# Kernel tuning notes

Hardware: AMD Instinct MI355X
Metric: run time of the kernel (lower is better)

## Reference

```python
import jax, jax.numpy as jnp
import numpy as np

# ---- dims ----
B, NP_, NL = 32, 350, 30          # graphs, protein atoms, ligand atoms per graph
NG = NP_ + NL
N = B * NG                        # 12160 nodes
E = B * NP_ * NL                  # 336000 edges (dense bipartite per graph)
HID, HEADS, G = 128, 16, 20
DH = HID // HEADS
KV = 2 * HID + G                  # 276
R_MIN, R_MAX = 0.0, 10.0


def _mlp_params(key, din, dout, hid=HID):
    k1, k2 = jax.random.split(key)
    return (jax.random.normal(k1, (din, hid), jnp.float32) / np.sqrt(din),
            jnp.zeros((hid,), jnp.float32),
            jnp.ones((hid,), jnp.float32),
            jnp.zeros((hid,), jnp.float32),
            jax.random.normal(k2, (hid, dout), jnp.float32) / np.sqrt(hid),
            jnp.zeros((dout,), jnp.float32))


def setup_inputs() -> dict:
    key = jax.random.key(0)
    h = jax.random.normal(jax.random.fold_in(key, 0), (N, HID), jnp.float32)
    x = jax.random.normal(jax.random.fold_in(key, 1), (N, 3), jnp.float32) * 3.0
    # node layout per graph: NP_ protein atoms then NL ligand atoms
    mask_ligand = np.tile(np.concatenate([np.zeros(NP_, np.int64), np.ones(NL, np.int64)]), B)
    base = (np.arange(B) * NG)[:, None]
    prot = base + np.arange(NP_)[None, :]            # [B, NP_]
    lig = base + NP_ + np.arange(NL)[None, :]        # [B, NL]
    # torch: dst = repeat_interleave(protein, NL); src = ligand.repeat(NP_)
    dst = np.repeat(prot, NL, axis=1).reshape(-1)
    src = np.tile(lig, (1, NP_)).reshape(-1)
    inp = {"h": h, "x": x, "src": jnp.asarray(src), "dst": jnp.asarray(dst),
           "mask_ligand": jnp.asarray(mask_ligand)}
    dims = {"hk": (KV, HID), "hv": (KV, HID), "xv": (KV, HEADS), "hq": (HID, HID), "no": (2 * HID, HID)}
    for i, (nm, (di, do)) in enumerate(dims.items()):
        for s, arr in zip(("w1", "b1", "g", "be", "w2", "b2"), _mlp_params(jax.random.fold_in(key, 10 + i), di, do)):
            inp[f"{nm}_{s}"] = arr
    return inp


def _mlp(t, w1, b1, g, be, w2, b2):
    # Linear -> LayerNorm -> ReLU -> Linear
    y = t @ w1 + b1
    mu = y.mean(-1, keepdims=True)
    var = ((y - mu) ** 2).mean(-1, keepdims=True)
    y = jax.nn.relu((y - mu) * jax.lax.rsqrt(var + 1e-5) * g + be)
    return y @ w2 + b2


def _forward(h, x, src, dst, mask_ligand, ps):
    rel_x = x[src] - x[dst]                                   # [E,3]
    dist = jnp.linalg.norm(rel_x, axis=-1, keepdims=True)     # [E,1]
    offset = jnp.linspace(R_MIN, R_MAX, G)
    coeff = -0.5 / (offset[1] - offset[0]) ** 2
    r_feat = jnp.exp(coeff * (dist - offset) ** 2)            # [E,G]; outer_product(v) == v
    # inner layer unpacks (dst_i, src_i) = (src, dst): hi=h[src_i]=h[dst], hj=h[dst_i]=h[src]
    kv = jnp.concatenate([r_feat, h[dst], h[src]], -1)        # [E,KV]
    k = _mlp(kv, *ps["hk"]).reshape(-1, HEADS, DH)            # [E,H,dh]
    q = _mlp(h, *ps["hq"]).reshape(-1, HEADS, DH)             # [N,H,dh]
    logits = (q[src] * k).sum(-1) / np.sqrt(DH)               # [E,H]
    # scatter_softmax over dst_i = src groups (ligand nodes)
    smax = jax.ops.segment_max(logits, src, num_segments=N)
    ex = jnp.exp(logits - smax[src])
    alpha = ex / jax.ops.segment_sum(ex, src, num_segments=N)[src]   # [E,H]
    v = _mlp(kv, *ps["hv"]).reshape(-1, HEADS, DH)            # [E,H,dh]
    xv = _mlp(kv, *ps["xv"])                                  # [E,H]
    m = alpha[:, :, None] * v                                 # [E,H,dh]
    mx = (alpha * xv)[:, :, None] * rel_x[:, None, :]         # [E,H,3]
    out = jax.ops.segment_sum(m, src, num_segments=N).reshape(N, HID)
    out_x = jax.ops.segment_sum(mx, src, num_segments=N)      # [N,H,3]
    # out_fc: h_in[mask_ligand] with int64 mask gathers rows 0/1 (faithful to source)
    out = _mlp(jnp.concatenate([out, h[mask_ligand]], -1), *ps["no"])
    h_out = out + h
    x_out = x + out_x.mean(1)
    return h_out, x_out


def reference(h, x, src, dst, mask_ligand,
              hk_w1, hk_b1, hk_g, hk_be, hk_w2, hk_b2,
              hv_w1, hv_b1, hv_g, hv_be, hv_w2, hv_b2,
              xv_w1, xv_b1, xv_g, xv_be, xv_w2, xv_b2,
              hq_w1, hq_b1, hq_g, hq_be, hq_w2, hq_b2,
              no_w1, no_b1, no_g, no_be, no_w2, no_b2):
    ps = {"hk": (hk_w1, hk_b1, hk_g, hk_be, hk_w2, hk_b2),
          "hv": (hv_w1, hv_b1, hv_g, hv_be, hv_w2, hv_b2),
          "xv": (xv_w1, xv_b1, xv_g, xv_be, xv_w2, xv_b2),
          "hq": (hq_w1, hq_b1, hq_g, hq_be, hq_w2, hq_b2),
          "no": (no_w1, no_b1, no_g, no_be, no_w2, no_b2)}
    return _forward(h, x, src, dst, mask_ligand, ps)
```

## Files before the change

kernel.cpp:

```cpp
#include <hip/hip_runtime.h>
#include <math.h>

namespace {
constexpr int kB = 32;
constexpr int kNP = 350;
constexpr int kNL = 30;
constexpr int kNG = 380;
constexpr int kN = kB * kNG;
constexpr int kG = 20;
constexpr int kNPROT = kB * kNP;
constexpr int kNLIG = kB * kNL;
constexpr int TP = 32;
constexpr int NT = 11;
}

__global__ __launch_bounds__(256) void pre_kernel(
    const float* __restrict__ h,
    const float* __restrict__ wk1, const float* __restrict__ bk1,
    const float* __restrict__ wv1, const float* __restrict__ bv1,
    const float* __restrict__ wx1, const float* __restrict__ bx1,
    float* __restrict__ outKd, float* __restrict__ outVd, float* __restrict__ outXd,
    float* __restrict__ outKs, float* __restrict__ outVs, float* __restrict__ outXs) {
  const int m = blockIdx.y;
  const float* w1 = (m == 0) ? wk1 : (m == 1) ? wv1 : wx1;
  const float* b1 = (m == 0) ? bk1 : (m == 1) ? bv1 : bx1;
  const bool isProt = (blockIdx.x < 175);
  const int rbase = isProt ? blockIdx.x * 64 : (blockIdx.x - 175) * 64;
  float* outArr = isProt ? ((m == 0) ? outKd : (m == 1) ? outVd : outXd)
                         : ((m == 0) ? outKs : (m == 1) ? outVs : outXs);
  const float* wb = w1 + (isProt ? 20 * 128 : 148 * 128);

  __shared__ float sh[64 * 132];
  const int t = threadIdx.x;
#pragma unroll
  for (int j = 0; j < 8; ++j) {
    int flat = t + j * 256;
    int row = flat >> 5;
    int col = (flat & 31) * 4;
    int r = rbase + row;
    int node;
    if (isProt) node = (r / kNP) * kNG + (r % kNP);
    else        node = (r / kNL) * kNG + kNP + (r % kNL);
    *(float4*)&sh[row * 132 + col] = *(const float4*)(h + (size_t)node * 128 + col);
  }
  __syncthreads();

  const int dcol = (t & 31) * 4;
  const int rrow = (t >> 5) * 8;
  float4 acc[8];
#pragma unroll
  for (int i = 0; i < 8; ++i) acc[i] = make_float4(0.f, 0.f, 0.f, 0.f);

  for (int k = 0; k < 128; k += 4) {
    float4 a4[8];
#pragma unroll
    for (int i = 0; i < 8; ++i) a4[i] = *(float4*)&sh[(rrow + i) * 132 + k];
#pragma unroll
    for (int kk = 0; kk < 4; ++kk) {
      float4 w4 = *(const float4*)(wb + (size_t)(k + kk) * 128 + dcol);
#pragma unroll
      for (int i = 0; i < 8; ++i) {
        float a = (kk == 0) ? a4[i].x : (kk == 1) ? a4[i].y : (kk == 2) ? a4[i].z : a4[i].w;
        acc[i].x += a * w4.x; acc[i].y += a * w4.y;
        acc[i].z += a * w4.z; acc[i].w += a * w4.w;
      }
    }
  }
  float4 bias = make_float4(0.f, 0.f, 0.f, 0.f);
  if (!isProt) bias = *(const float4*)(b1 + dcol);
#pragma unroll
  for (int i = 0; i < 8; ++i) {
    float4 o = acc[i];
    o.x += bias.x; o.y += bias.y; o.z += bias.z; o.w += bias.w;
    *(float4*)(outArr + (size_t)(rbase + rrow + i) * 128 + dcol) = o;
  }
}

__global__ __launch_bounds__(128) void cvec_kernel(
    const float* __restrict__ h,
    const float* __restrict__ no_w1, const float* __restrict__ no_b1,
    const float* __restrict__ no_g, const float* __restrict__ no_be,
    const float* __restrict__ no_w2, const float* __restrict__ no_b2,
    float* __restrict__ cvec) {
  __shared__ float sy[128];
  __shared__ float sa[128];
  __shared__ float red[2];
  const int d = threadIdx.x;
  float y = no_b1[d];
  for (int i = 0; i < 128; ++i) y += h[i] * no_w1[(size_t)(128 + i) * 128 + d];
  sy[d] = y;
  __syncthreads();
  if (d == 0) {
    float s = 0.f, ss = 0.f;
    for (int i = 0; i < 128; ++i) { s += sy[i]; ss += sy[i] * sy[i]; }
    float mu = s / 128.f;
    red[0] = mu;
    red[1] = rsqrtf(ss / 128.f - mu * mu + 1e-5f);
  }
  __syncthreads();
  float a = (y - red[0]) * red[1] * no_g[d] + no_be[d];
  sa[d] = fmaxf(a, 0.f);
  __syncthreads();
  float o = no_b2[d];
  for (int i = 0; i < 128; ++i) o += sa[i] * no_w2[(size_t)i * 128 + d];
  cvec[d] = o;
}

__global__ __launch_bounds__(256) void prot_kernel(
    const float* __restrict__ h, const float* __restrict__ x,
    const float* __restrict__ cvec, float* __restrict__ hout, float* __restrict__ xout) {
  int idx = blockIdx.x * 256 + threadIdx.x;
  if (idx < kNPROT * 32) {
    int r = idx >> 5, c4 = (idx & 31) * 4;
    int node = (r / kNP) * kNG + (r % kNP);
    float4 hv = *(const float4*)(h + (size_t)node * 128 + c4);
    float4 cv = *(const float4*)(cvec + c4);
    *(float4*)(hout + (size_t)node * 128 + c4) =
        make_float4(hv.x + cv.x, hv.y + cv.y, hv.z + cv.z, hv.w + cv.w);
  }
  if (idx < kNPROT * 3) {
    int r = idx / 3, c = idx % 3;
    int node = (r / kNP) * kNG + (r % kNP);
    xout[(size_t)node * 3 + c] = x[(size_t)node * 3 + c];
  }
}

struct W20 {
  float4 a0, a1, a2, a3, a4, a5, a6, a7, a8, a9;
  float4 a10, a11, a12, a13, a14, a15, a16, a17, a18, a19;
};

__device__ __forceinline__ W20 load_w20(const float* __restrict__ W, int c4) {
  W20 r;
  r.a0  = *(const float4*)(W + 0 * 128 + c4);
  r.a1  = *(const float4*)(W + 1 * 128 + c4);
  r.a2  = *(const float4*)(W + 2 * 128 + c4);
  r.a3  = *(const float4*)(W + 3 * 128 + c4);
  r.a4  = *(const float4*)(W + 4 * 128 + c4);
  r.a5  = *(const float4*)(W + 5 * 128 + c4);
  r.a6  = *(const float4*)(W + 6 * 128 + c4);
  r.a7  = *(const float4*)(W + 7 * 128 + c4);
  r.a8  = *(const float4*)(W + 8 * 128 + c4);
  r.a9  = *(const float4*)(W + 9 * 128 + c4);
  r.a10 = *(const float4*)(W + 10 * 128 + c4);
  r.a11 = *(const float4*)(W + 11 * 128 + c4);
  r.a12 = *(const float4*)(W + 12 * 128 + c4);
  r.a13 = *(const float4*)(W + 13 * 128 + c4);
  r.a14 = *(const float4*)(W + 14 * 128 + c4);
  r.a15 = *(const float4*)(W + 15 * 128 + c4);
  r.a16 = *(const float4*)(W + 16 * 128 + c4);
  r.a17 = *(const float4*)(W + 17 * 128 + c4);
  r.a18 = *(const float4*)(W + 18 * 128 + c4);
  r.a19 = *(const float4*)(W + 19 * 128 + c4);
  return r;
}

__device__ __forceinline__ float4 gemm20(const W20& w, const float* rfp, float4 yv) {
  const float4 ra = *(const float4*)(rfp + 0);
  const float4 rb = *(const float4*)(rfp + 4);
  const float4 rc = *(const float4*)(rfp + 8);
  const float4 rd = *(const float4*)(rfp + 12);
  const float4 re = *(const float4*)(rfp + 16);
  yv.x += ra.x * w.a0.x;  yv.y += ra.x * w.a0.y;  yv.z += ra.x * w.a0.z;  yv.w += ra.x * w.a0.w;
  yv.x += ra.y * w.a1.x;  yv.y += ra.y * w.a1.y;  yv.z += ra.y * w.a1.z;  yv.w += ra.y * w.a1.w;
  yv.x += ra.z * w.a2.x;  yv.y += ra.z * w.a2.y;  yv.z += ra.z * w.a2.z;  yv.w += ra.z * w.a2.w;
  yv.x += ra.w * w.a3.x;  yv.y += ra.w * w.a3.y;  yv.z += ra.w * w.a3.z;  yv.w += ra.w * w.a3.w;
  yv.x += rb.x * w.a4.x;  yv.y += rb.x * w.a4.y;  yv.z += rb.x * w.a4.z;  yv.w += rb.x * w.a4.w;
  yv.x += rb.y * w.a5.x;  yv.y += rb.y * w.a5.y;  yv.z += rb.y * w.a5.z;  yv.w += rb.y * w.a5.w;
  yv.x += rb.z * w.a6.x;  yv.y += rb.z * w.a6.y;  yv.z += rb.z * w.a6.z;  yv.w += rb.z * w.a6.w;
  yv.x += rb.w * w.a7.x;  yv.y += rb.w * w.a7.y;  yv.z += rb.w * w.a7.z;  yv.w += rb.w * w.a7.w;
  yv.x += rc.x * w.a8.x;  yv.y += rc.x * w.a8.y;  yv.z += rc.x * w.a8.z;  yv.w += rc.x * w.a8.w;
  yv.x += rc.y * w.a9.x;  yv.y += rc.y * w.a9.y;  yv.z += rc.y * w.a9.z;  yv.w += rc.y * w.a9.w;
  yv.x += rc.z * w.a10.x; yv.y += rc.z * w.a10.y; yv.z += rc.z * w.a10.z; yv.w += rc.z * w.a10.w;
  yv.x += rc.w * w.a11.x; yv.y += rc.w * w.a11.y; yv.z += rc.w * w.a11.z; yv.w += rc.w * w.a11.w;
  yv.x += rd.x * w.a12.x; yv.y += rd.x * w.a12.y; yv.z += rd.x * w.a12.z; yv.w += rd.x * w.a12.w;
  yv.x += rd.y * w.a13.x; yv.y += rd.y * w.a13.y; yv.z += rd.y * w.a13.z; yv.w += rd.y * w.a13.w;
  yv.x += rd.z * w.a14.x; yv.y += rd.z * w.a14.y; yv.z += rd.z * w.a14.z; yv.w += rd.z * w.a14.w;
  yv.x += rd.w * w.a15.x; yv.y += rd.w * w.a15.y; yv.z += rd.w * w.a15.z; yv.w += rd.w * w.a15.w;
  yv.x += re.x * w.a16.x; yv.y += re.x * w.a16.y; yv.z += re.x * w.a16.z; yv.w += re.x * w.a16.w;
  yv.x += re.y * w.a17.x; yv.y += re.y * w.a17.y; yv.z += re.y * w.a17.z; yv.w += re.y * w.a17.w;
  yv.x += re.z * w.a18.x; yv.y += re.z * w.a18.y; yv.z += re.z * w.a18.z; yv.w += re.z * w.a18.w;
  yv.x += re.w * w.a19.x; yv.y += re.w * w.a19.y; yv.z += re.w * w.a19.z; yv.w += re.w * w.a19.w;
  return yv;
}

__device__ __forceinline__ void ln_relu_store(float4 yv, float4 g4, float4 be4, float* dst) {
  float s = yv.x + yv.y + yv.z + yv.w;
  float ss = yv.x * yv.x + yv.y * yv.y + yv.z * yv.z + yv.w * yv.w;
  for (int m = 16; m; m >>= 1) { s += __shfl_xor(s, m); ss += __shfl_xor(ss, m); }
  float mu = s * (1.f / 128.f);
  float rs = rsqrtf(ss * (1.f / 128.f) - mu * mu + 1e-5f);
  float4 a;
  a.x = fmaxf((yv.x - mu) * rs * g4.x + be4.x, 0.f);
  a.y = fmaxf((yv.y - mu) * rs * g4.y + be4.y, 0.f);
  a.z = fmaxf((yv.z - mu) * rs * g4.z + be4.z, 0.f);
  a.w = fmaxf((yv.w - mu) * rs * g4.w + be4.w, 0.f);
  *(float4*)dst = a;
}

__device__ __forceinline__ float4 addf4(float4 a, float4 b) {
  return make_float4(a.x + b.x, a.y + b.y, a.z + b.z, a.w + b.w);
}

__global__ __launch_bounds__(256, 2) void edge_kernel(
    const float* __restrict__ h, const float* __restrict__ x,
    const float* __restrict__ preKd, const float* __restrict__ preVd, const float* __restrict__ preXd,
    const float* __restrict__ preKs, const float* __restrict__ preVs, const float* __restrict__ preXs,
    const float* __restrict__ hk_w1, const float* __restrict__ hk_g, const float* __restrict__ hk_be,
    const float* __restrict__ hk_w2, const float* __restrict__ hk_b2,
    const float* __restrict__ hv_w1, const float* __restrict__ hv_g, const float* __restrict__ hv_be,
    const float* __restrict__ hv_w2, const float* __restrict__ hv_b2,
    const float* __restrict__ xv_w1, const float* __restrict__ xv_g, const float* __restrict__ xv_be,
    const float* __restrict__ xv_w2, const float* __restrict__ xv_b2,
    const float* __restrict__ hq_w1, const float* __restrict__ hq_b1, const float* __restrict__ hq_g,
    const float* __restrict__ hq_be, const float* __restrict__ hq_w2, const float* __restrict__ hq_b2,
    const float* __restrict__ no_w1, const float* __restrict__ no_b1, const float* __restrict__ no_g,
    const float* __restrict__ no_be, const float* __restrict__ no_w2, const float* __restrict__ no_b2,
    float* __restrict__ hout, float* __restrict__ xout) {

  __shared__ float smem[13236];
  float* const s_qw    = smem;
  float* const s_logit = smem + 2112;
  float* const s_a     = smem + 7712;
  float* const s_rfu   = smem + 11936;
  float* const s_q     = s_rfu;
  float* const s_outv  = s_rfu + 128;
  float* const s_outx  = s_rfu + 256;
  float* const s_dist  = smem + 12576;
  float* const s_tmp   = smem + 12928;
  float* const s_qb    = smem + 13184;
  float* const s_mx    = smem + 13200;
  float* const s_sum   = smem + 13216;
  float* const s_red   = smem + 13232;

  const int wg = blockIdx.x;
  const int g = wg / kNL, l = wg % kNL;
  const int lignode = g * kNG + kNP + l;
  const int ligidx = g * kNL + l;
  const int t = threadIdx.x;
  const int c4 = (t & 31) * 4;
  const int myp = t >> 5;

  constexpr float kStep = 10.f / 19.f;
  constexpr float kCoeff = -0.5f / (kStep * kStep);

  const float lx0 = x[(size_t)lignode * 3 + 0];
  const float lx1 = x[(size_t)lignode * 3 + 1];
  const float lx2 = x[(size_t)lignode * 3 + 2];

  if (t < 32) *(float4*)&s_tmp[t * 4] = *(const float4*)(h + (size_t)lignode * 128 + t * 4);
  for (int p = t; p < kNP; p += 256) {
    const float* xp = x + (size_t)(g * kNG + p) * 3;
    float r0 = lx0 - xp[0], r1 = lx1 - xp[1], r2 = lx2 - xp[2];
    s_dist[p] = sqrtf(r0 * r0 + r1 * r1 + r2 * r2);
  }
  __syncthreads();

  float yq = 0.f;
  if (t < 128) {
    yq = hq_b1[t];
    for (int k = 0; k < 128; ++k) yq += s_tmp[k] * hq_w1[(size_t)k * 128 + t];
    s_a[t] = yq;
  }
  __syncthreads();
  if (t < 64) {
    float v0 = s_a[t], v1 = s_a[t + 64];
    float s = v0 + v1, ss = v0 * v0 + v1 * v1;
#pragma unroll
    for (int off = 32; off; off >>= 1) { s += __shfl_xor(s, off); ss += __shfl_xor(ss, off); }
    if (t == 0) {
      float mu = s / 128.f;
      s_red[0] = mu;
      s_red[1] = rsqrtf(ss / 128.f - mu * mu + 1e-5f);
    }
  }
  __syncthreads();
  if (t < 128) {
    float a = (yq - s_red[0]) * s_red[1] * hq_g[t] + hq_be[t];
    s_tmp[t] = fmaxf(a, 0.f);
  }
  __syncthreads();
  if (t < 128) {
    float qv = hq_b2[t];
    for (int d = 0; d < 128; ++d) qv += s_tmp[d] * hq_w2[(size_t)d * 128 + t];
    s_q[t] = qv;
  }
  __syncthreads();

  constexpr float kInvSqrtDH = 0.35355339059327379f;
#pragma unroll
  for (int i = 0; i < 8; ++i) {
    int idx = t + i * 256;
    int hh = idx >> 7, d = idx & 127;
    float4 wa = *(const float4*)(hk_w2 + (size_t)d * 128 + hh * 8);
    float4 wb = *(const float4*)(hk_w2 + (size_t)d * 128 + hh * 8 + 4);
    float v = wa.x * s_q[hh * 8 + 0] + wa.y * s_q[hh * 8 + 1] + wa.z * s_q[hh * 8 + 2] +
              wa.w * s_q[hh * 8 + 3] + wb.x * s_q[hh * 8 + 4] + wb.y * s_q[hh * 8 + 5] +
              wb.z * s_q[hh * 8 + 6] + wb.w * s_q[hh * 8 + 7];
    s_qw[hh * 132 + d] = v * kInvSqrtDH;
  }
  if (t < 16) {
    float v = 0.f;
#pragma unroll
    for (int j = 0; j < 8; ++j) v += hk_b2[t * 8 + j] * s_q[t * 8 + j];
    s_qb[t] = v * kInvSqrtDH;
  }
  for (int o = t; o < TP * 20; o += 256) {
    int p = o / 20;
    float dd = s_dist[p] - (o - p * 20) * kStep;
    s_rfu[o] = __expf(kCoeff * dd * dd);
  }
  __syncthreads();

  {
    const W20 w = load_w20(hk_w1, c4);
    const float4 g4 = *(const float4*)(hk_g + c4);
    const float4 be4 = *(const float4*)(hk_be + c4);
    const float4 pres4 = *(const float4*)(preKs + (size_t)ligidx * 128 + c4);

    for (int tile = 0; tile < NT; ++tile) {
      const int p0 = tile * TP;
      const int np = (350 - p0) < TP ? (350 - p0) : TP;
      const int i0 = myp, i1 = myp + 8, i2 = myp + 16, i3 = myp + 24;
      float4 pr0, pr1, pr2, pr3;
      const float* base = preKd + (size_t)(g * kNP + p0) * 128 + c4;
      pr0 = *(const float4*)(base + (size_t)i0 * 128);
      pr1 = *(const float4*)(base + (size_t)i1 * 128);
      pr2 = *(const float4*)(base + (size_t)i2 * 128);
      if (i3 < np) pr3 = *(const float4*)(base + (size_t)i3 * 128);
      ln_relu_store(gemm20(w, &s_rfu[i0 * 20], addf4(pres4, pr0)), g4, be4, &s_a[i0 * 132 + c4]);
      ln_relu_store(gemm20(w, &s_rfu[i1 * 20], addf4(pres4, pr1)), g4, be4, &s_a[i1 * 132 + c4]);
      ln_relu_store(gemm20(w, &s_rfu[i2 * 20], addf4(pres4, pr2)), g4, be4, &s_a[i2 * 132 + c4]);
      if (i3 < np)
        ln_relu_store(gemm20(w, &s_rfu[i3 * 20], addf4(pres4, pr3)), g4, be4, &s_a[i3 * 132 + c4]);
      __syncthreads();
      {
        const int p = t & 31;
        const int h0 = (t >> 5) * 2, h1 = h0 + 1;
        float f0 = 0.f, f1 = 0.f;
#pragma unroll
        for (int d = 0; d < 128; d += 4) {
          float4 a4 = *(float4*)&s_a[p * 132 + d];
          float4 q0 = *(float4*)&s_qw[h0 * 132 + d];
          float4 q1 = *(float4*)&s_qw[h1 * 132 + d];
          f0 += a4.x * q0.x + a4.y * q0.y + a4.z * q0.z + a4.w * q0.w;
          f1 += a4.x * q1.x + a4.y * q1.y + a4.z * q1.z + a4.w * q1.w;
        }
        if (p < np) {
          s_logit[(p0 + p) * 16 + h0] = f0 + s_qb[h0];
          s_logit[(p0 + p) * 16 + h1] = f1 + s_qb[h1];
        }
        const int nxt = (tile + 1 == NT) ? 0 : tile + 1;
        const int q0p = nxt * TP;
        const int nq = (350 - q0p) < TP ? (350 - q0p) : TP;
        for (int o = t; o < nq * 20; o += 256) {
          int pp = o / 20;
          float dd = s_dist[q0p + pp] - (o - pp * 20) * kStep;
          s_rfu[o] = __expf(kCoeff * dd * dd);
        }
      }
      __syncthreads();
    }
  }

  {
    int hh = t & 15, ck = t >> 4;
    float mx = -1e30f;
    for (int p = ck; p < 350; p += 16) mx = fmaxf(mx, s_logit[p * 16 + hh]);
    s_tmp[t] = mx;
  }
  __syncthreads();
  if (t < 16) {
    float mx = s_tmp[t];
    for (int c = 1; c < 16; ++c) mx = fmaxf(mx, s_tmp[c * 16 + t]);
    s_mx[t] = mx;
  }
  __syncthreads();
  {
    int hh = t & 15, ck = t >> 4;
    float mx = s_mx[hh], sm = 0.f;
    for (int p = ck; p < 350; p += 16) sm += __expf(s_logit[p * 16 + hh] - mx);
    s_tmp[t] = sm;
  }
  __syncthreads();
  if (t < 16) {
    float sm = 0.f;
    for (int c = 0; c < 16; ++c) sm += s_tmp[c * 16 + t];
    s_sum[t] = 1.f / sm;
  }
  __syncthreads();
  for (int o = t; o < 350 * 16; o += 256) {
    int hh = o & 15;
    s_logit[o] = __expf(s_logit[o] - s_mx[hh]) * s_sum[hh];
  }
  for (int o = t; o < 2048; o += 256) {
    int hh = o >> 7, d = o & 127;
    s_qw[hh * 132 + d] = xv_w2[(size_t)d * 16 + hh];
  }
  if (t < 16) s_qb[t] = xv_b2[t];
  __syncthreads();

  float accv0 = 0.f, accv1 = 0.f, accv2 = 0.f, accv3 = 0.f;
  float accv4 = 0.f, accv5 = 0.f, accv6 = 0.f, accv7 = 0.f;
  const int dd_ = t & 127;
  const int hb8 = (t >> 7) * 8;
  {
    const W20 w = load_w20(hv_w1, c4);
    const float4 g4 = *(const float4*)(hv_g + c4);
    const float4 be4 = *(const float4*)(hv_be + c4);
    const float4 pres4 = *(const float4*)(preVs + (size_t)ligidx * 128 + c4);

    for (int tile = 0; tile < NT; ++tile) {
      const int p0 = tile * TP;
      const int np = (350 - p0) < TP ? (350 - p0) : TP;
      const int i0 = myp, i1 = myp + 8, i2 = myp + 16, i3 = myp + 24;
      float4 pr0, pr1, pr2, pr3;
      const float* base = preVd + (size_t)(g * kNP + p0) * 128 + c4;
      pr0 = *(const float4*)(base + (size_t)i0 * 128);
      pr1 = *(const float4*)(base + (size_t)i1 * 128);
      pr2 = *(const float4*)(base + (size_t)i2 * 128);
      if (i3 < np) pr3 = *(const float4*)(base + (size_t)i3 * 128);
      ln_relu_store(gemm20(w, &s_rfu[i0 * 20], addf4(pres4, pr0)), g4, be4, &s_a[i0 * 132 + c4]);
      ln_relu_store(gemm20(w, &s_rfu[i1 * 20], addf4(pres4, pr1)), g4, be4, &s_a[i1 * 132 + c4]);
      ln_relu_store(gemm20(w, &s_rfu[i2 * 20], addf4(pres4, pr2)), g4, be4, &s_a[i2 * 132 + c4]);
      if (i3 < np)
        ln_relu_store(gemm20(w, &s_rfu[i3 * 20], addf4(pres4, pr3)), g4, be4, &s_a[i3 * 132 + c4]);
      __syncthreads();
      for (int p = 0; p < np; ++p) {
        float av = s_a[p * 132 + dd_];
        float4 alA = *(float4*)&s_logit[(p0 + p) * 16 + hb8];
        float4 alB = *(float4*)&s_logit[(p0 + p) * 16 + hb8 + 4];
        accv0 += alA.x * av; accv1 += alA.y * av;
        accv2 += alA.z * av; accv3 += alA.w * av;
        accv4 += alB.x * av; accv5 += alB.y * av;
        accv6 += alB.z * av; accv7 += alB.w * av;
      }
      {
        const int nxt = (tile + 1 == NT) ? 0 : tile + 1;
        const int q0p = nxt * TP;
        const int nq = (350 - q0p) < TP ? (350 - q0p) : TP;
        for (int o = t; o < nq * 20; o += 256) {
          int pp = o / 20;
          float dd2 = s_dist[q0p + pp] - (o - pp * 20) * kStep;
          s_rfu[o] = __expf(kCoeff * dd2 * dd2);
        }
      }
      __syncthreads();
    }
  }

  float ax0 = 0.f, ax1 = 0.f, ax2 = 0.f, ax3 = 0.f, ax4 = 0.f, ax5 = 0.f;
  {
    const W20 w = load_w20(xv_w1, c4);
    const float4 g4 = *(const float4*)(xv_g + c4);
    const float4 be4 = *(const float4*)(xv_be + c4);
    const float4 pres4 = *(const float4*)(preXs + (size_t)ligidx * 128 + c4);
    const int p_ = t & 31;
    const int h0 = (t >> 5) * 2, h1 = h0 + 1;

    for (int tile = 0; tile < NT; ++tile) {
      const int p0 = tile * TP;
      const int np = (350 - p0) < TP ? (350 - p0) : TP;
      const int i0 = myp, i1 = myp + 8, i2 = myp + 16, i3 = myp + 24;
      float4 pr0, pr1, pr2, pr3;
      const float* base = preXd + (size_t)(g * kNP + p0) * 128 + c4;
      pr0 = *(const float4*)(base + (size_t)i0 * 128);
      pr1 = *(const float4*)(base + (size_t)i1 * 128);
      pr2 = *(const float4*)(base + (size_t)i2 * 128);
      if (i3 < np) pr3 = *(const float4*)(base + (size_t)i3 * 128);
      ln_relu_store(gemm20(w, &s_rfu[i0 * 20], addf4(pres4, pr0)), g4, be4, &s_a[i0 * 132 + c4]);
      ln_relu_store(gemm20(w, &s_rfu[i1 * 20], addf4(pres4, pr1)), g4, be4, &s_a[i1 * 132 + c4]);
      ln_relu_store(gemm20(w, &s_rfu[i2 * 20], addf4(pres4, pr2)), g4, be4, &s_a[i2 * 132 + c4]);
      if (i3 < np)
        ln_relu_store(gemm20(w, &s_rfu[i3 * 20], addf4(pres4, pr3)), g4, be4, &s_a[i3 * 132 + c4]);
      __syncthreads();
      {
        float f0 = 0.f, f1 = 0.f;
#pragma unroll
        for (int d = 0; d < 128; d += 4) {
          float4 a4 = *(float4*)&s_a[p_ * 132 + d];
          float4 q0 = *(float4*)&s_qw[h0 * 132 + d];
          float4 q1 = *(float4*)&s_qw[h1 * 132 + d];
          f0 += a4.x * q0.x + a4.y * q0.y + a4.z * q0.z + a4.w * q0.w;
          f1 += a4.x * q1.x + a4.y * q1.y + a4.z * q1.z + a4.w * q1.w;
        }
        float w0 = 0.f, w1 = 0.f, r0 = 0.f, r1 = 0.f, r2 = 0.f;
        if (p_ < np) {
          int pg = p0 + p_;
          w0 = s_logit[pg * 16 + h0] * (f0 + s_qb[h0]);
          w1 = s_logit[pg * 16 + h1] * (f1 + s_qb[h1]);
          const float* xp = x + (size_t)(g * kNG + pg) * 3;
          r0 = lx0 - xp[0]; r1 = lx1 - xp[1]; r2 = lx2 - xp[2];
        }
        float p00 = w0 * r0, p01 = w0 * r1, p02 = w0 * r2;
        float p10 = w1 * r0, p11 = w1 * r1, p12 = w1 * r2;
#pragma unroll
        for (int m = 16; m; m >>= 1) {
          p00 += __shfl_xor(p00, m); p01 += __shfl_xor(p01, m); p02 += __shfl_xor(p02, m);
          p10 += __shfl_xor(p10, m); p11 += __shfl_xor(p11, m); p12 += __shfl_xor(p12, m);
        }
        ax0 += p00; ax1 += p01; ax2 += p02;
        ax3 += p10; ax4 += p11; ax5 += p12;
      }
      {
        const int nxt = (tile + 1 == NT) ? 0 : tile + 1;
        const int q0p = nxt * TP;
        const int nq = (350 - q0p) < TP ? (350 - q0p) : TP;
        for (int o = t; o < nq * 20; o += 256) {
          int pp = o / 20;
          float dd2 = s_dist[q0p + pp] - (o - pp * 20) * kStep;
          s_rfu[o] = __expf(kCoeff * dd2 * dd2);
        }
      }
      __syncthreads();
    }
  }

  s_a[(hb8 + 0) * 132 + dd_] = accv0;
  s_a[(hb8 + 1) * 132 + dd_] = accv1;
  s_a[(hb8 + 2) * 132 + dd_] = accv2;
  s_a[(hb8 + 3) * 132 + dd_] = accv3;
  s_a[(hb8 + 4) * 132 + dd_] = accv4;
  s_a[(hb8 + 5) * 132 + dd_] = accv5;
  s_a[(hb8 + 6) * 132 + dd_] = accv6;
  s_a[(hb8 + 7) * 132 + dd_] = accv7;
  {
    const int h0 = (t >> 5) * 2;
    if ((t & 31) == 0) {
      s_outx[h0 * 4 + 0] = ax0; s_outx[h0 * 4 + 1] = ax1; s_outx[h0 * 4 + 2] = ax2;
      s_outx[(h0 + 1) * 4 + 0] = ax3; s_outx[(h0 + 1) * 4 + 1] = ax4;
      s_outx[(h0 + 1) * 4 + 2] = ax5;
    }
  }
  __syncthreads();

  if (t < 128) {
    float o = hv_b2[t];
    const int hh = t >> 3;
    for (int d = 0; d < 128; ++d) o += s_a[hh * 132 + d] * hv_w2[(size_t)d * 128 + t];
    s_outv[t] = o;
  }
  if (t >= 128 && t < 131) {
    int c = t - 128;
    float sm = 0.f;
#pragma unroll
    for (int hh = 0; hh < 16; ++hh) sm += s_outx[hh * 4 + c];
    xout[(size_t)lignode * 3 + c] = x[(size_t)lignode * 3 + c] + sm * (1.f / 16.f);
  }
  __syncthreads();
  float yn = 0.f;
  if (t < 128) {
    yn = no_b1[t];
    for (int i = 0; i < 128; ++i) yn += s_outv[i] * no_w1[(size_t)i * 128 + t];
    const float* h1 = h + 128;
    for (int i = 0; i < 128; ++i) yn += h1[i] * no_w1[(size_t)(128 + i) * 128 + t];
    s_tmp[t] = yn;
  }
  __syncthreads();
  if (t < 64) {
    float v0 = s_tmp[t], v1 = s_tmp[t + 64];
    float s = v0 + v1, ss = v0 * v0 + v1 * v1;
#pragma unroll
    for (int off = 32; off; off >>= 1) { s += __shfl_xor(s, off); ss += __shfl_xor(ss, off); }
    if (t == 0) {
      float mu = s / 128.f;
      s_red[0] = mu;
      s_red[1] = rsqrtf(ss / 128.f - mu * mu + 1e-5f);
    }
  }
  __syncthreads();
  if (t < 128) {
    float a = (yn - s_red[0]) * s_red[1] * no_g[t] + no_be[t];
    s_outv[t] = fmaxf(a, 0.f);
  }
  __syncthreads();
  if (t < 128) {
    float o = no_b2[t];
    for (int d = 0; d < 128; ++d) o += s_outv[d] * no_w2[(size_t)d * 128 + t];
    hout[(size_t)lignode * 128 + t] = o + h[(size_t)lignode * 128 + t];
  }
}

extern "C" void kernel_launch(void* const* d_in, const int* in_sizes, int n_in,
                              void* d_out, int out_size, void* d_ws, size_t ws_size,
                              hipStream_t stream) {
  (void)in_sizes; (void)n_in; (void)out_size; (void)ws_size;
  const float* h = (const float*)d_in[0];
  const float* x = (const float*)d_in[1];
  const float* hk_w1 = (const float*)d_in[5];
  const float* hk_b1 = (const float*)d_in[6];
  const float* hk_g  = (const float*)d_in[7];
  const float* hk_be = (const float*)d_in[8];
  const float* hk_w2 = (const float*)d_in[9];
  const float* hk_b2 = (const float*)d_in[10];
  const float* hv_w1 = (const float*)d_in[11];
  const float* hv_b1 = (const float*)d_in[12];
  const float* hv_g  = (const float*)d_in[13];
  const float* hv_be = (const float*)d_in[14];
  const float* hv_w2 = (const float*)d_in[15];
  const float* hv_b2 = (const float*)d_in[16];
  const float* xv_w1 = (const float*)d_in[17];
  const float* xv_b1 = (const float*)d_in[18];
  const float* xv_g  = (const float*)d_in[19];
  const float* xv_be = (const float*)d_in[20];
  const float* xv_w2 = (const float*)d_in[21];
  const float* xv_b2 = (const float*)d_in[22];
  const float* hq_w1 = (const float*)d_in[23];
  const float* hq_b1 = (const float*)d_in[24];
  const float* hq_g  = (const float*)d_in[25];
  const float* hq_be = (const float*)d_in[26];
  const float* hq_w2 = (const float*)d_in[27];
  const float* hq_b2 = (const float*)d_in[28];
  const float* no_w1 = (const float*)d_in[29];
  const float* no_b1 = (const float*)d_in[30];
  const float* no_g  = (const float*)d_in[31];
  const float* no_be = (const float*)d_in[32];
  const float* no_w2 = (const float*)d_in[33];
  const float* no_b2 = (const float*)d_in[34];

  float* ws = (float*)d_ws;
  float* preKd = ws;
  float* preVd = preKd + (size_t)kNPROT * 128;
  float* preXd = preVd + (size_t)kNPROT * 128;
  float* preKs = preXd + (size_t)kNPROT * 128;
  float* preVs = preKs + (size_t)kNLIG * 128;
  float* preXs = preVs + (size_t)kNLIG * 128;
  float* cvec  = preXs + (size_t)kNLIG * 128;

  float* hout = (float*)d_out;
  float* xout = hout + (size_t)kN * 128;

  pre_kernel<<<dim3(190, 3), dim3(256), 0, stream>>>(
      h, hk_w1, hk_b1, hv_w1, hv_b1, xv_w1, xv_b1,
      preKd, preVd, preXd, preKs, preVs, preXs);
  cvec_kernel<<<dim3(1), dim3(128), 0, stream>>>(
      h, no_w1, no_b1, no_g, no_be, no_w2, no_b2, cvec);
  edge_kernel<<<dim3(960), dim3(256), 0, stream>>>(
      h, x, preKd, preVd, preXd, preKs, preVs, preXs,
      hk_w1, hk_g, hk_be, hk_w2, hk_b2,
      hv_w1, hv_g, hv_be, hv_w2, hv_b2,
      xv_w1, xv_g, xv_be, xv_w2, xv_b2,
      hq_w1, hq_b1, hq_g, hq_be, hq_w2, hq_b2,
      no_w1, no_b1, no_g, no_be, no_w2, no_b2,
      hout, xout);
  prot_kernel<<<dim3(1400), dim3(256), 0, stream>>>(h, x, cvec, hout, xout);
}
```

Measured before the change: 694.7 us.

## Remap edge MLP first layer to 2 columns per thread, raise occupancy to 3

The per-edge first-layer GEMM+LayerNorm now has each thread own 2 of the 128 hidden columns instead of 4, with a full 64-lane wavefront covering one row. The cached weight slice shrinks from 80 to 40 registers, and the launch bound moves from 2 to 3 blocks per SM to use the freed registers. In exchange, each wave processes 8 rows sequentially with a 6-step shuffle reduction in place of the 5-step one, so instruction-level parallelism from the unrolled 4-row batch is lost. An extra barrier was also added before the RBF precompute.

```diff
diff --git a/kernel.cpp b/kernel.cpp
--- a/kernel.cpp
+++ b/kernel.cpp
@@ -125,84 +125,78 @@
   }
 }
 
-struct W20 {
-  float4 a0, a1, a2, a3, a4, a5, a6, a7, a8, a9;
-  float4 a10, a11, a12, a13, a14, a15, a16, a17, a18, a19;
+struct W20h {
+  float2 b0, b1, b2, b3, b4, b5, b6, b7, b8, b9;
+  float2 b10, b11, b12, b13, b14, b15, b16, b17, b18, b19;
 };
 
-__device__ __forceinline__ W20 load_w20(const float* __restrict__ W, int c4) {
-  W20 r;
-  r.a0  = *(const float4*)(W + 0 * 128 + c4);
-  r.a1  = *(const float4*)(W + 1 * 128 + c4);
-  r.a2  = *(const float4*)(W + 2 * 128 + c4);
-  r.a3  = *(const float4*)(W + 3 * 128 + c4);
-  r.a4  = *(const float4*)(W + 4 * 128 + c4);
-  r.a5  = *(const float4*)(W + 5 * 128 + c4);
-  r.a6  = *(const float4*)(W + 6 * 128 + c4);
-  r.a7  = *(const float4*)(W + 7 * 128 + c4);
-  r.a8  = *(const float4*)(W + 8 * 128 + c4);
-  r.a9  = *(const float4*)(W + 9 * 128 + c4);
-  r.a10 = *(const float4*)(W + 10 * 128 + c4);
-  r.a11 = *(const float4*)(W + 11 * 128 + c4);
-  r.a12 = *(const float4*)(W + 12 * 128 + c4);
-  r.a13 = *(const float4*)(W + 13 * 128 + c4);
-  r.a14 = *(const float4*)(W + 14 * 128 + c4);
-  r.a15 = *(const float4*)(W + 15 * 128 + c4);
-  r.a16 = *(const float4*)(W + 16 * 128 + c4);
-  r.a17 = *(const float4*)(W + 17 * 128 + c4);
-  r.a18 = *(const float4*)(W + 18 * 128 + c4);
-  r.a19 = *(const float4*)(W + 19 * 128 + c4);
+__device__ __forceinline__ W20h load_w20h(const float* __restrict__ W, int c2) {
+  W20h r;
+  r.b0  = *(const float2*)(W + 0 * 128 + c2);
+  r.b1  = *(const float2*)(W + 1 * 128 + c2);
+  r.b2  = *(const float2*)(W + 2 * 128 + c2);
+  r.b3  = *(const float2*)(W + 3 * 128 + c2);
+  r.b4  = *(const float2*)(W + 4 * 128 + c2);
+  r.b5  = *(const float2*)(W + 5 * 128 + c2);
+  r.b6  = *(const float2*)(W + 6 * 128 + c2);
+  r.b7  = *(const float2*)(W + 7 * 128 + c2);
+  r.b8  = *(const float2*)(W + 8 * 128 + c2);
+  r.b9  = *(const float2*)(W + 9 * 128 + c2);
+  r.b10 = *(const float2*)(W + 10 * 128 + c2);
+  r.b11 = *(const float2*)(W + 11 * 128 + c2);
+  r.b12 = *(const float2*)(W + 12 * 128 + c2);
+  r.b13 = *(const float2*)(W + 13 * 128 + c2);
+  r.b14 = *(const float2*)(W + 14 * 128 + c2);
+  r.b15 = *(const float2*)(W + 15 * 128 + c2);
+  r.b16 = *(const float2*)(W + 16 * 128 + c2);
+  r.b17 = *(const float2*)(W + 17 * 128 + c2);
+  r.b18 = *(const float2*)(W + 18 * 128 + c2);
+  r.b19 = *(const float2*)(W + 19 * 128 + c2);
   return r;
 }
 
-__device__ __forceinline__ float4 gemm20(const W20& w, const float* rfp, float4 yv) {
+__device__ __forceinline__ float2 gemm20h(const W20h& w, const float* rfp, float2 yv) {
   const float4 ra = *(const float4*)(rfp + 0);
   const float4 rb = *(const float4*)(rfp + 4);
   const float4 rc = *(const float4*)(rfp + 8);
   const float4 rd = *(const float4*)(rfp + 12);
   const float4 re = *(const float4*)(rfp + 16);
-  yv.x += ra.x * w.a0.x;  yv.y += ra.x * w.a0.y;  yv.z += ra.x * w.a0.z;  yv.w += ra.x * w.a0.w;
-  yv.x += ra.y * w.a1.x;  yv.y += ra.y * w.a1.y;  yv.z += ra.y * w.a1.z;  yv.w += ra.y * w.a1.w;
-  yv.x += ra.z * w.a2.x;  yv.y += ra.z * w.a2.y;  yv.z += ra.z * w.a2.z;  yv.w += ra.z * w.a2.w;
-  yv.x += ra.w * w.a3.x;  yv.y += ra.w * w.a3.y;  yv.z += ra.w * w.a3.z;  yv.w += ra.w * w.a3.w;
-  yv.x += rb.x * w.a4.x;  yv.y += rb.x * w.a4.y;  yv.z += rb.x * w.a4.z;  yv.w += rb.x * w.a4.w;
-  yv.x += rb.y * w.a5.x;  yv.y += rb.y * w.a5.y;  yv.z += rb.y * w.a5.z;  yv.w += rb.y * w.a5.w;
-  yv.x += rb.z * w.a6.x;  yv.y += rb.z * w.a6.y;  yv.z += rb.z * w.a6.z;  yv.w += rb.z * w.a6.w;
-  yv.x += rb.w * w.a7.x;  yv.y += rb.w * w.a7.y;  yv.z += rb.w * w.a7.z;  yv.w += rb.w * w.a7.w;
-  yv.x += rc.x * w.a8.x;  yv.y += rc.x * w.a8.y;  yv.z += rc.x * w.a8.z;  yv.w += rc.x * w.a8.w;
-  yv.x += rc.y * w.a9.x;  yv.y += rc.y * w.a9.y;  yv.z += rc.y * w.a9.z;  yv.w += rc.y * w.a9.w;
-  yv.x += rc.z * w.a10.x; yv.y += rc.z * w.a10.y; yv.z += rc.z * w.a10.z; yv.w += rc.z * w.a10.w;
-  yv.x += rc.w * w.a11.x; yv.y += rc.w * w.a11.y; yv.z += rc.w * w.a11.z; yv.w += rc.w * w.a11.w;
-  yv.x += rd.x * w.a12.x; yv.y += rd.x * w.a12.y; yv.z += rd.x * w.a12.z; yv.w += rd.x * w.a12.w;
-  yv.x += rd.y * w.a13.x; yv.y += rd.y * w.a13.y; yv.z += rd.y * w.a13.z; yv.w += rd.y * w.a13.w;
-  yv.x += rd.z * w.a14.x; yv.y += rd.z * w.a14.y; yv.z += rd.z * w.a14.z; yv.w += rd.z * w.a14.w;
-  yv.x += rd.w * w.a15.x; yv.y += rd.w * w.a15.y; yv.z += rd.w * w.a15.z; yv.w += rd.w * w.a15.w;
-  yv.x += re.x * w.a16.x; yv.y += re.x * w.a16.y; yv.z += re.x * w.a16.z; yv.w += re.x * w.a16.w;
-  yv.x += re.y * w.a17.x; yv.y += re.y * w.a17.y; yv.z += re.y * w.a17.z; yv.w += re.y * w.a17.w;
-  yv.x += re.z * w.a18.x; yv.y += re.z * w.a18.y; yv.z += re.z * w.a18.z; yv.w += re.z * w.a18.w;
-  yv.x += re.w * w.a19.x; yv.y += re.w * w.a19.y; yv.z += re.w * w.a19.z; yv.w += re.w * w.a19.w;
+  yv.x += ra.x * w.b0.x;  yv.y += ra.x * w.b0.y;
+  yv.x += ra.y * w.b1.x;  yv.y += ra.y * w.b1.y;
+  yv.x += ra.z * w.b2.x;  yv.y += ra.z * w.b2.y;
+  yv.x += ra.w * w.b3.x;  yv.y += ra.w * w.b3.y;
+  yv.x += rb.x * w.b4.x;  yv.y += rb.x * w.b4.y;
+  yv.x += rb.y * w.b5.x;  yv.y += rb.y * w.b5.y;
+  yv.x += rb.z * w.b6.x;  yv.y += rb.z * w.b6.y;
+  yv.x += rb.w * w.b7.x;  yv.y += rb.w * w.b7.y;
+  yv.x += rc.x * w.b8.x;  yv.y += rc.x * w.b8.y;
+  yv.x += rc.y * w.b9.x;  yv.y += rc.y * w.b9.y;
+  yv.x += rc.z * w.b10.x; yv.y += rc.z * w.b10.y;
+  yv.x += rc.w * w.b11.x; yv.y += rc.w * w.b11.y;
+  yv.x += rd.x * w.b12.x; yv.y += rd.x * w.b12.y;
+  yv.x += rd.y * w.b13.x; yv.y += rd.y * w.b13.y;
+  yv.x += rd.z * w.b14.x; yv.y += rd.z * w.b14.y;
+  yv.x += rd.w * w.b15.x; yv.y += rd.w * w.b15.y;
+  yv.x += re.x * w.b16.x; yv.y += re.x * w.b16.y;
+  yv.x += re.y * w.b17.x; yv.y += re.y * w.b17.y;
+  yv.x += re.z * w.b18.x; yv.y += re.z * w.b18.y;
+  yv.x += re.w * w.b19.x; yv.y += re.w * w.b19.y;
   return yv;
 }
 
-__device__ __forceinline__ void ln_relu_store(float4 yv, float4 g4, float4 be4, float* dst) {
-  float s = yv.x + yv.y + yv.z + yv.w;
-  float ss = yv.x * yv.x + yv.y * yv.y + yv.z * yv.z + yv.w * yv.w;
-  for (int m = 16; m; m >>= 1) { s += __shfl_xor(s, m); ss += __shfl_xor(ss, m); }
+__device__ __forceinline__ void ln2_relu_store(float2 yv, float2 g2, float2 be2, float* dst) {
+  float s = yv.x + yv.y;
+  float ss = yv.x * yv.x + yv.y * yv.y;
+  for (int m = 32; m; m >>= 1) { s += __shfl_xor(s, m); ss += __shfl_xor(ss, m); }
   float mu = s * (1.f / 128.f);
   float rs = rsqrtf(ss * (1.f / 128.f) - mu * mu + 1e-5f);
-  float4 a;
-  a.x = fmaxf((yv.x - mu) * rs * g4.x + be4.x, 0.f);
-  a.y = fmaxf((yv.y - mu) * rs * g4.y + be4.y, 0.f);
-  a.z = fmaxf((yv.z - mu) * rs * g4.z + be4.z, 0.f);
-  a.w = fmaxf((yv.w - mu) * rs * g4.w + be4.w, 0.f);
-  *(float4*)dst = a;
-}
-
-__device__ __forceinline__ float4 addf4(float4 a, float4 b) {
-  return make_float4(a.x + b.x, a.y + b.y, a.z + b.z, a.w + b.w);
-}
-
-__global__ __launch_bounds__(256, 2) void edge_kernel(
+  float2 a;
+  a.x = fmaxf((yv.x - mu) * rs * g2.x + be2.x, 0.f);
+  a.y = fmaxf((yv.y - mu) * rs * g2.y + be2.y, 0.f);
+  *(float2*)dst = a;
+}
+
+__global__ __launch_bounds__(256, 3) void edge_kernel(
     const float* __restrict__ h, const float* __restrict__ x,
     const float* __restrict__ preKd, const float* __restrict__ preVd, const float* __restrict__ preXd,
     const float* __restrict__ preKs, const float* __restrict__ preVs, const float* __restrict__ preXs,
@@ -238,8 +232,8 @@
   const int lignode = g * kNG + kNP + l;
   const int ligidx = g * kNL + l;
   const int t = threadIdx.x;
-  const int c4 = (t & 31) * 4;
-  const int myp = t >> 5;
+  const int c2 = (t & 63) * 2;
+  const int wv = t >> 6;
 
   constexpr float kStep = 10.f / 19.f;
   constexpr float kCoeff = -0.5f / (kStep * kStep);
@@ -305,6 +299,7 @@
     for (int j = 0; j < 8; ++j) v += hk_b2[t * 8 + j] * s_q[t * 8 + j];
     s_qb[t] = v * kInvSqrtDH;
   }
+  __syncthreads();
   for (int o = t; o < TP * 20; o += 256) {
     int p = o / 20;
     float dd = s_dist[p] - (o - p * 20) * kStep;
@@ -313,26 +308,24 @@
   __syncthreads();
 
   {
-    const W20 w = load_w20(hk_w1, c4);
-    const float4 g4 = *(const float4*)(hk_g + c4);
-    const float4 be4 = *(const float4*)(hk_be + c4);
-    const float4 pres4 = *(const float4*)(preKs + (size_t)ligidx * 128 + c4);
+    const W20h w = load_w20h(hk_w1, c2);
+    const float2 g2 = *(const float2*)(hk_g + c2);
+    const float2 be2 = *(const float2*)(hk_be + c2);
+    const float2 pres2 = *(const float2*)(preKs + (size_t)ligidx * 128 + c2);
 
     for (int tile = 0; tile < NT; ++tile) {
       const int p0 = tile * TP;
       const int np = (350 - p0) < TP ? (350 - p0) : TP;
-      const int i0 = myp, i1 = myp + 8, i2 = myp + 16, i3 = myp + 24;
-      float4 pr0, pr1, pr2, pr3;
-      const float* base = preKd + (size_t)(g * kNP + p0) * 128 + c4;
-      pr0 = *(const float4*)(base + (size_t)i0 * 128);
-      pr1 = *(const float4*)(base + (size_t)i1 * 128);
-      pr2 = *(const float4*)(base + (size_t)i2 * 128);
-      if (i3 < np) pr3 = *(const float4*)(base + (size_t)i3 * 128);
-      ln_relu_store(gemm20(w, &s_rfu[i0 * 20], addf4(pres4, pr0)), g4, be4, &s_a[i0 * 132 + c4]);
-      ln_relu_store(gemm20(w, &s_rfu[i1 * 20], addf4(pres4, pr1)), g4, be4, &s_a[i1 * 132 + c4]);
-      ln_relu_store(gemm20(w, &s_rfu[i2 * 20], addf4(pres4, pr2)), g4, be4, &s_a[i2 * 132 + c4]);
-      if (i3 < np)
-        ln_relu_store(gemm20(w, &s_rfu[i3 * 20], addf4(pres4, pr3)), g4, be4, &s_a[i3 * 132 + c4]);
+      const float* base = preKd + (size_t)(g * kNP + p0) * 128 + c2;
+      for (int r = 0; r < 8; ++r) {
+        const int row = wv * 8 + r;
+        if (row < np) {
+          float2 pr = *(const float2*)(base + (size_t)row * 128);
+          float2 yv = make_float2(pres2.x + pr.x, pres2.y + pr.y);
+          yv = gemm20h(w, &s_rfu[row * 20], yv);
+          ln2_relu_store(yv, g2, be2, &s_a[row * 132 + c2]);
+        }
+      }
       __syncthreads();
       {
         const int p = t & 31;
@@ -405,26 +398,24 @@
   const int dd_ = t & 127;
   const int hb8 = (t >> 7) * 8;
   {
-    const W20 w = load_w20(hv_w1, c4);
-    const float4 g4 = *(const float4*)(hv_g + c4);
-    const float4 be4 = *(const float4*)(hv_be + c4);
-    const float4 pres4 = *(const float4*)(preVs + (size_t)ligidx * 128 + c4);
+    const W20h w = load_w20h(hv_w1, c2);
+    const float2 g2 = *(const float2*)(hv_g + c2);
+    const float2 be2 = *(const float2*)(hv_be + c2);
+    const float2 pres2 = *(const float2*)(preVs + (size_t)ligidx * 128 + c2);
 
     for (int tile = 0; tile < NT; ++tile) {
       const int p0 = tile * TP;
       const int np = (350 - p0) < TP ? (350 - p0) : TP;
-      const int i0 = myp, i1 = myp + 8, i2 = myp + 16, i3 = myp + 24;
-      float4 pr0, pr1, pr2, pr3;
-      const float* base = preVd + (size_t)(g * kNP + p0) * 128 + c4;
-      pr0 = *(const float4*)(base + (size_t)i0 * 128);
-      pr1 = *(const float4*)(base + (size_t)i1 * 128);
-      pr2 = *(const float4*)(base + (size_t)i2 * 128);
-      if (i3 < np) pr3 = *(const float4*)(base + (size_t)i3 * 128);
-      ln_relu_store(gemm20(w, &s_rfu[i0 * 20], addf4(pres4, pr0)), g4, be4, &s_a[i0 * 132 + c4]);
-      ln_relu_store(gemm20(w, &s_rfu[i1 * 20], addf4(pres4, pr1)), g4, be4, &s_a[i1 * 132 + c4]);
-      ln_relu_store(gemm20(w, &s_rfu[i2 * 20], addf4(pres4, pr2)), g4, be4, &s_a[i2 * 132 + c4]);
-      if (i3 < np)
-        ln_relu_store(gemm20(w, &s_rfu[i3 * 20], addf4(pres4, pr3)), g4, be4, &s_a[i3 * 132 + c4]);
+      const float* base = preVd + (size_t)(g * kNP + p0) * 128 + c2;
+      for (int r = 0; r < 8; ++r) {
+        const int row = wv * 8 + r;
+        if (row < np) {
+          float2 pr = *(const float2*)(base + (size_t)row * 128);
+          float2 yv = make_float2(pres2.x + pr.x, pres2.y + pr.y);
+          yv = gemm20h(w, &s_rfu[row * 20], yv);
+          ln2_relu_store(yv, g2, be2, &s_a[row * 132 + c2]);
+        }
+      }
       __syncthreads();
       for (int p = 0; p < np; ++p) {
         float av = s_a[p * 132 + dd_];
@@ -451,28 +442,26 @@
 
   float ax0 = 0.f, ax1 = 0.f, ax2 = 0.f, ax3 = 0.f, ax4 = 0.f, ax5 = 0.f;
   {
-    const W20 w = load_w20(xv_w1, c4);
-    const float4 g4 = *(const float4*)(xv_g + c4);
-    const float4 be4 = *(const float4*)(xv_be + c4);
-    const float4 pres4 = *(const float4*)(preXs + (size_t)ligidx * 128 + c4);
+    const W20h w = load_w20h(xv_w1, c2);
+    const float2 g2 = *(const float2*)(xv_g + c2);
+    const float2 be2 = *(const float2*)(xv_be + c2);
+    const float2 pres2 = *(const float2*)(preXs + (size_t)ligidx * 128 + c2);
     const int p_ = t & 31;
     const int h0 = (t >> 5) * 2, h1 = h0 + 1;
 
     for (int tile = 0; tile < NT; ++tile) {
       const int p0 = tile * TP;
       const int np = (350 - p0) < TP ? (350 - p0) : TP;
-      const int i0 = myp, i1 = myp + 8, i2 = myp + 16, i3 = myp + 24;
-      float4 pr0, pr1, pr2, pr3;
-      const float* base = preXd + (size_t)(g * kNP + p0) * 128 + c4;
-      pr0 = *(const float4*)(base + (size_t)i0 * 128);
-      pr1 = *(const float4*)(base + (size_t)i1 * 128);
-      pr2 = *(const float4*)(base + (size_t)i2 * 128);
-      if (i3 < np) pr3 = *(const float4*)(base + (size_t)i3 * 128);
-      ln_relu_store(gemm20(w, &s_rfu[i0 * 20], addf4(pres4, pr0)), g4, be4, &s_a[i0 * 132 + c4]);
-      ln_relu_store(gemm20(w, &s_rfu[i1 * 20], addf4(pres4, pr1)), g4, be4, &s_a[i1 * 132 + c4]);
-      ln_relu_store(gemm20(w, &s_rfu[i2 * 20], addf4(pres4, pr2)), g4, be4, &s_a[i2 * 132 + c4]);
-      if (i3 < np)
-        ln_relu_store(gemm20(w, &s_rfu[i3 * 20], addf4(pres4, pr3)), g4, be4, &s_a[i3 * 132 + c4]);
+      const float* base = preXd + (size_t)(g * kNP + p0) * 128 + c2;
+      for (int r = 0; r < 8; ++r) {
+        const int row = wv * 8 + r;
+        if (row < np) {
+          float2 pr = *(const float2*)(base + (size_t)row * 128);
+          float2 yv = make_float2(pres2.x + pr.x, pres2.y + pr.y);
+          yv = gemm20h(w, &s_rfu[row * 20], yv);
+          ln2_relu_store(yv, g2, be2, &s_a[row * 132 + c2]);
+        }
+      }
       __syncthreads();
       {
         float f0 = 0.f, f1 = 0.f;
```

Measured after the change: 888.5 us. +27.9%, slower.
